# Kernel tuning notes

Measured on AMD Instinct MI355X. Metric: run time of the kernel, lower is better.

The kernel has to match this reference:

```python
import jax, jax.numpy as jnp
import numpy as np

N_ATOMS = 64
NC2 = N_ATOMS * (N_ATOMS - 1) // 2  # 2016
BATCH = 32768


def setup_inputs() -> dict:
    key = jax.random.key(0)
    decompFE = jax.random.normal(key, (BATCH, NC2), dtype=jnp.float32)
    return {"decompFE": decompFE}


def reference(decompFE):
    # Flat NC2 values map to strict lower triangle positions in row-major
    # order: (1,0),(2,0),(2,1),(3,0),... which is exactly jnp.tril_indices(n,-1).
    b, nc2 = decompFE.shape
    n = N_ATOMS
    rows, cols = jnp.tril_indices(n, k=-1)  # each length NC2, row-major order
    # Scatter flat values into strict lower triangle of [b, n, n]
    lower = jnp.zeros((b, n, n), dtype=decompFE.dtype).at[:, rows, cols].set(decompFE)
    # Symmetrize (diagonal stays zero)
    return lower + jnp.swapaxes(lower, -1, -2)
```

## Files before the change

### kernel.cpp

```cpp
#include <hip/hip_runtime.h>

constexpr int N_ATOMS = 64;
constexpr int NC2 = N_ATOMS * (N_ATOMS - 1) / 2;
constexpr int BATCH = 32768;

__global__ __launch_bounds__(256) void triangle_kernel(
    const float* __restrict__ in, float* __restrict__ out) {
    __shared__ float sm[NC2];

    const int b = blockIdx.x;
    const int t = threadIdx.x;

    const float4* in4 = reinterpret_cast<const float4*>(in + (size_t)b * NC2);
    float4* sm4 = reinterpret_cast<float4*>(sm);
#pragma unroll
    for (int it = 0; it < 2; ++it) {
        int idx = it * 256 + t;
        if (idx < NC2 / 4) {
            sm4[idx] = in4[idx];
        }
    }
    __syncthreads();

    float4* out4 = reinterpret_cast<float4*>(out + (size_t)b * N_ATOMS * N_ATOMS);
#pragma unroll
    for (int it = 0; it < 4; ++it) {
        int e4 = it * 256 + t;
        int e = e4 * 4;
        int i = e >> 6;
        int j0 = e & 63;

        int base_lower = i * (i - 1) / 2;

        float vv[4];
#pragma unroll
        for (int k = 0; k < 4; ++k) {
            int j = j0 + k;
            float val;
            if (j < i) {
                val = sm[base_lower + j];
            } else if (j > i) {
                val = sm[j * (j - 1) / 2 + i];
            } else {
                val = 0.0f;
            }
            vv[k] = val;
        }
        out4[e4] = make_float4(vv[0], vv[1], vv[2], vv[3]);
    }
}

extern "C" void kernel_launch(void* const* d_in, const int* in_sizes, int n_in,
                              void* d_out, int out_size, void* d_ws, size_t ws_size,
                              hipStream_t stream) {
    const float* in = (const float*)d_in[0];
    float* out = (float*)d_out;
    triangle_kernel<<<BATCH, 256, 0, stream>>>(in, out);
}
```

Baseline: 675.4 us.

## Process eight rows per block with double-buffered async global-to-LDS staging

Each block now handles eight batch rows instead of one. While the current row is gathered from shared memory and written out, the next row is streamed into a second LDS buffer with global_load_lds, using explicit vmcnt waits and barriers. The source indices for the symmetric gather are computed once per thread and reused for all eight rows, and a zero sentinel in LDS replaces the diagonal branch. This is meant to hide load latency and cut per-block launch and index overhead, at the cost of fragile hand-written waitcnt logic and fewer blocks in the grid.

```diff
diff --git a/kernel.cpp b/kernel.cpp
--- a/kernel.cpp
+++ b/kernel.cpp
@@ -1,52 +1,90 @@
 #include <hip/hip_runtime.h>
+#include <stdint.h>
 
 constexpr int N_ATOMS = 64;
 constexpr int NC2 = N_ATOMS * (N_ATOMS - 1) / 2;
 constexpr int BATCH = 32768;
+constexpr int ROWS_PER_BLOCK = 8;
+constexpr int NBLOCKS = BATCH / ROWS_PER_BLOCK;
+constexpr int BUF_FLOATS = 2048;
+
+__device__ __forceinline__ void stage_chunk16(const float* g, float* l) {
+    __builtin_amdgcn_global_load_lds(
+        (const __attribute__((address_space(1))) void*)g,
+        (__attribute__((address_space(3))) void*)l, 16, 0, 0);
+}
 
 __global__ __launch_bounds__(256) void triangle_kernel(
     const float* __restrict__ in, float* __restrict__ out) {
-    __shared__ float sm[NC2];
+    __shared__ __align__(16) float sm[2][BUF_FLOATS];
 
-    const int b = blockIdx.x;
     const int t = threadIdx.x;
 
-    const float4* in4 = reinterpret_cast<const float4*>(in + (size_t)b * NC2);
-    float4* sm4 = reinterpret_cast<float4*>(sm);
+    if (t == 0) {
+        sm[0][2016] = 0.0f;
+        sm[1][2016] = 0.0f;
+    }
+
+    int srcB[16];
 #pragma unroll
-    for (int it = 0; it < 2; ++it) {
-        int idx = it * 256 + t;
-        if (idx < NC2 / 4) {
-            sm4[idx] = in4[idx];
+    for (int it = 0; it < 4; ++it) {
+        const int e4 = it * 256 + t;
+        const int e = e4 * 4;
+        const int i = e >> 6;
+        const int j0 = e & 63;
+        const int bl = i * (i - 1) / 2;
+#pragma unroll
+        for (int k = 0; k < 4; ++k) {
+            const int j = j0 + k;
+            int s;
+            if (j < i)      s = bl + j;
+            else if (j > i) s = j * (j - 1) / 2 + i;
+            else            s = 2016;
+            srcB[it * 4 + k] = s * 4;
         }
     }
+
+    const int b0 = blockIdx.x * ROWS_PER_BLOCK;
+    const float* rowPtr = in + (size_t)b0 * NC2;
+
+    stage_chunk16(rowPtr + 4 * t,         &sm[0][0] + 4 * t);
+    stage_chunk16(rowPtr + 4 * (248 + t), &sm[0][0] + 4 * (248 + t));
     __syncthreads();
 
-    float4* out4 = reinterpret_cast<float4*>(out + (size_t)b * N_ATOMS * N_ATOMS);
 #pragma unroll
-    for (int it = 0; it < 4; ++it) {
-        int e4 = it * 256 + t;
-        int e = e4 * 4;
-        int i = e >> 6;
-        int j0 = e & 63;
+    for (int k = 0; k < ROWS_PER_BLOCK; ++k) {
+        if (k + 1 < ROWS_PER_BLOCK) {
+            const float* nxt = rowPtr + NC2;
+            float* dst = &sm[(k + 1) & 1][0];
+            stage_chunk16(nxt + 4 * t,         dst + 4 * t);
+            stage_chunk16(nxt + 4 * (248 + t), dst + 4 * (248 + t));
+        }
 
-        int base_lower = i * (i - 1) / 2;
+        if (k > 0) {
+            if (k + 1 < ROWS_PER_BLOCK) {
+                asm volatile("s_waitcnt vmcnt(6)" ::: "memory");
+            } else {
+                asm volatile("s_waitcnt vmcnt(4)" ::: "memory");
+            }
+            __builtin_amdgcn_s_barrier();
+            __builtin_amdgcn_sched_barrier(0);
+        }
 
-        float vv[4];
+        const char* sbase = (const char*)(&sm[k & 1][0]);
+        float4* out4 = reinterpret_cast<float4*>(out + (size_t)(b0 + k) * (N_ATOMS * N_ATOMS));
 #pragma unroll
-        for (int k = 0; k < 4; ++k) {
-            int j = j0 + k;
-            float val;
-            if (j < i) {
-                val = sm[base_lower + j];
-            } else if (j > i) {
-                val = sm[j * (j - 1) / 2 + i];
-            } else {
-                val = 0.0f;
-            }
-            vv[k] = val;
+        for (int it = 0; it < 4; ++it) {
+            const float v0 = *(const float*)(sbase + srcB[it * 4 + 0]);
+            const float v1 = *(const float*)(sbase + srcB[it * 4 + 1]);
+            const float v2 = *(const float*)(sbase + srcB[it * 4 + 2]);
+            const float v3 = *(const float*)(sbase + srcB[it * 4 + 3]);
+            out4[it * 256 + t] = make_float4(v0, v1, v2, v3);
         }
-        out4[e4] = make_float4(vv[0], vv[1], vv[2], vv[3]);
+
+        if (k + 1 < ROWS_PER_BLOCK) {
+            __builtin_amdgcn_s_barrier();
+        }
+        rowPtr += NC2;
     }
 }
 
@@ -55,5 +93,5 @@
                               hipStream_t stream) {
     const float* in = (const float*)d_in[0];
     float* out = (float*)d_out;
-    triangle_kernel<<<BATCH, 256, 0, stream>>>(in, out);
+    triangle_kernel<<<NBLOCKS, 256, 0, stream>>>(in, out);
 }
```

Result: no change. 687.9 us (+1.8%).

## Stage input rows via direct global-to-LDS loads with 512-thread blocks

Applied to the files above, without the earlier changes.

Replaces the register-staged float4 copy into shared memory with __builtin_amdgcn_global_load_lds, which writes 16-byte chunks straight into LDS. The block grows to 512 threads so each thread issues one chunk. The last 8 threads redundantly reload earlier chunks to avoid divergence. The diagonal now reads a zero sentinel at sm[2016] instead of branching to a constant, and the block writes its output in two passes. The aim is to cut VGPR round-trips and instruction overhead in a memory-bound kernel. The risks are reliance on builtin support for 16-byte LDS loads and the ordering between the sentinel store and the async loads.

```diff
diff --git a/kernel.cpp b/kernel.cpp
--- a/kernel.cpp
+++ b/kernel.cpp
@@ -4,49 +4,47 @@
 constexpr int NC2 = N_ATOMS * (N_ATOMS - 1) / 2;
 constexpr int BATCH = 32768;
 
-__global__ __launch_bounds__(256) void triangle_kernel(
+__device__ __forceinline__ void stage_chunk16(const float* g, float* l) {
+    __builtin_amdgcn_global_load_lds(
+        (const __attribute__((address_space(1))) void*)g,
+        (__attribute__((address_space(3))) void*)l, 16, 0, 0);
+}
+
+__global__ __launch_bounds__(512) void triangle_kernel(
     const float* __restrict__ in, float* __restrict__ out) {
-    __shared__ float sm[NC2];
+    __shared__ __align__(16) float sm[2048];
 
+    const int t = threadIdx.x;
     const int b = blockIdx.x;
-    const int t = threadIdx.x;
 
-    const float4* in4 = reinterpret_cast<const float4*>(in + (size_t)b * NC2);
-    float4* sm4 = reinterpret_cast<float4*>(sm);
-#pragma unroll
-    for (int it = 0; it < 2; ++it) {
-        int idx = it * 256 + t;
-        if (idx < NC2 / 4) {
-            sm4[idx] = in4[idx];
-        }
-    }
+    if (t == 0) sm[2016] = 0.0f;
+
+    const float* row = in + (size_t)b * NC2;
+    const int c = (t < 448) ? t : (t - 8);
+    stage_chunk16(row + 4 * c, &sm[4 * c]);
+
     __syncthreads();
 
-    float4* out4 = reinterpret_cast<float4*>(out + (size_t)b * N_ATOMS * N_ATOMS);
+    float4* out4 = reinterpret_cast<float4*>(out + (size_t)b * (N_ATOMS * N_ATOMS));
 #pragma unroll
-    for (int it = 0; it < 4; ++it) {
-        int e4 = it * 256 + t;
-        int e = e4 * 4;
-        int i = e >> 6;
-        int j0 = e & 63;
+    for (int half = 0; half < 2; ++half) {
+        const int e4 = half * 512 + t;
+        const int e = e4 * 4;
+        const int i = e >> 6;
+        const int j0 = e & 63;
+        const int bl = i * (i - 1) / 2;
 
-        int base_lower = i * (i - 1) / 2;
-
-        float vv[4];
+        float v[4];
 #pragma unroll
         for (int k = 0; k < 4; ++k) {
-            int j = j0 + k;
-            float val;
-            if (j < i) {
-                val = sm[base_lower + j];
-            } else if (j > i) {
-                val = sm[j * (j - 1) / 2 + i];
-            } else {
-                val = 0.0f;
-            }
-            vv[k] = val;
+            const int j = j0 + k;
+            int s;
+            if (j < i)      s = bl + j;
+            else if (j > i) s = j * (j - 1) / 2 + i;
+            else            s = 2016;
+            v[k] = sm[s];
         }
-        out4[e4] = make_float4(vv[0], vv[1], vv[2], vv[3]);
+        out4[e4] = make_float4(v[0], v[1], v[2], v[3]);
     }
 }
 
@@ -55,5 +53,5 @@
                               hipStream_t stream) {
     const float* in = (const float*)d_in[0];
     float* out = (float*)d_out;
-    triangle_kernel<<<BATCH, 256, 0, stream>>>(in, out);
+    triangle_kernel<<<BATCH, 512, 0, stream>>>(in, out);
 }
```

After: 671.3 us. No clear change (-0.6%).
